# Optimization experiments

Hardware: AMD Instinct MI355X
Metric: run time of the kernel (lower is better)

## Reference

```python
import jax, jax.numpy as jnp
import numpy as np

S, B, C, H, M = 384, 8, 1024, 16, 1536
CC = C // H


def setup_inputs() -> dict:
    key = jax.random.key(0)
    ks = jax.random.split(key, 8)
    x = jax.random.normal(ks[0], (S, B, C), dtype=jnp.float32)
    pe = jax.random.normal(ks[1], (S, B, C), dtype=jnp.float32)
    memory_k = jax.random.normal(ks[2], (M, B, H, CC), dtype=jnp.float32)
    memory_v = jax.random.normal(ks[3], (M, B, H, CC), dtype=jnp.float32)
    w_qkv = jax.random.normal(ks[4], (C, 3 * C), dtype=jnp.float32) * 0.02
    b_qkv = jnp.zeros((3 * C,), dtype=jnp.float32)
    w_out = jax.random.normal(ks[5], (C, C), dtype=jnp.float32) * 0.02
    b_out = jnp.zeros((C,), dtype=jnp.float32)
    terminal = jnp.zeros((B,), dtype=bool)
    # causal mask over the new tokens: True = masked (future positions)
    content_mask = jnp.broadcast_to(
        (jnp.arange(S)[None, :] > jnp.arange(S)[:, None])[:, :, None], (S, S, B))
    padding_mask = jnp.zeros((S, B), dtype=bool)  # True = padded
    memory_length = jax.random.randint(ks[6], (B,), 0, M, dtype=jnp.int32)
    return dict(x=x, positional_encoding=pe, memory_k=memory_k, memory_v=memory_v,
                w_qkv=w_qkv, b_qkv=b_qkv, w_out=w_out, b_out=b_out,
                terminal=terminal, content_mask=content_mask,
                padding_mask=padding_mask, memory_length=memory_length)


def reference(x, positional_encoding, memory_k, memory_v, w_qkv, b_qkv,
              w_out, b_out, terminal, content_mask, padding_mask, memory_length):
    s, b, c = x.shape
    # qkv projection
    qkv = (x + positional_encoding) @ w_qkv + b_qkv          # [s,b,3c]
    q, k, v = jnp.split(qkv, 3, axis=-1)
    q = q.reshape(s, b, H, CC)
    k = k.reshape(s, b, H, CC)
    v = v.reshape(s, b, H, CC)
    # clear_memory(terminal): zero lengths for terminal episodes
    mem_len = jnp.where(terminal, 0, memory_length)          # [b]
    # ragged memory concat expressed with fixed capacity M + padding mask
    k_full = jnp.concatenate([memory_k, k], axis=0)          # [M+s,b,H,CC]
    v_full = jnp.concatenate([memory_v, v], axis=0)
    mem_pad = jnp.arange(M)[:, None] >= mem_len[None, :]     # [M,b] True=masked
    kv_pad = jnp.concatenate([mem_pad, padding_mask], axis=0)  # [M+s,b]
    mem_content = jnp.zeros((s, M, b), dtype=bool)           # memory visible to all queries
    full_content = jnp.concatenate([mem_content, content_mask], axis=1)  # [s,M+s,b]
    mask = full_content | kv_pad[None, :, :]                 # [s,M+s,b]
    # attention
    scores = jnp.einsum('sbhc,tbhc->stbh', q, k_full) * (1.0 / np.sqrt(CC))
    scores = jnp.where(mask[:, :, :, None], jnp.float32(-1e9), scores)
    p = jax.nn.softmax(scores, axis=1)                       # [s,M+s,b,h]
    out = jnp.einsum('stbh,tbhc->sbhc', p, v_full).reshape(s, b, c)
    return out @ w_out + b_out
```

## Files before the change

### kernel.cpp

```cpp
#include <hip/hip_runtime.h>
#include <math.h>

#define S_DIM 384
#define B_DIM 8
#define C_DIM 1024
#define H_DIM 16
#define M_DIM 1536
#define CC_DIM 64
#define ROWS  (S_DIM * B_DIM)
#define N3C   (3 * C_DIM)
#define NSPLIT 4

typedef unsigned short u16;
typedef short bf8v  __attribute__((ext_vector_type(8)));
typedef short bf4v  __attribute__((ext_vector_type(4)));
typedef u16   us8   __attribute__((ext_vector_type(8)));
typedef u16   us4   __attribute__((ext_vector_type(4)));
typedef float f4v   __attribute__((ext_vector_type(4)));

__device__ __forceinline__ u16 f2bf(float f) {
    unsigned u = __float_as_uint(f);
    u += 0x7fffu + ((u >> 16) & 1u);
    return (u16)(u >> 16);
}
__device__ __forceinline__ float bf2f(u16 v) {
    return __uint_as_float(((unsigned)v) << 16);
}
#if __has_builtin(__builtin_amdgcn_exp2f)
#define EX2(x) __builtin_amdgcn_exp2f(x)
#else
#define EX2(x) __expf((x) * 0.69314718056f)
#endif
#define QSCALE (0.125f * 1.44269504f)

__device__ __forceinline__ f4v mfma16x16x16bf16(bf4v a, bf4v b, f4v c) {
#if __has_builtin(__builtin_amdgcn_mfma_f32_16x16x16bf16_1k)
    return __builtin_amdgcn_mfma_f32_16x16x16bf16_1k(a, b, c, 0, 0, 0);
#else
    return c;
#endif
}

__device__ __forceinline__ void gload16(const u16* g, u16* l) {
    __builtin_amdgcn_global_load_lds(
        (const __attribute__((address_space(1))) void*)g,
        (__attribute__((address_space(3))) void*)l, 16, 0, 0);
}

__device__ __forceinline__ void tr32(const float* __restrict__ in, u16* __restrict__ out,
                                     int R, int Cc, int r0, int c0, int tid, float* sm) {
    #pragma unroll
    for (int i = 0; i < 4; i++) {
        int r = i * 8 + (tid >> 5), c = tid & 31;
        sm[r * 33 + c] = in[(size_t)(r0 + r) * Cc + c0 + c];
    }
    __syncthreads();
    #pragma unroll
    for (int i = 0; i < 4; i++) {
        int cw = i * 8 + (tid >> 5), rw = tid & 31;
        out[(size_t)(c0 + cw) * R + r0 + rw] = f2bf(sm[rw * 33 + cw]);
    }
}

__global__ __launch_bounds__(256) void prep_all(
    const float* __restrict__ x, const float* __restrict__ pe, u16* __restrict__ Abf,
    const float* __restrict__ wqkv, u16* __restrict__ Wqkvt,
    const float* __restrict__ wout, u16* __restrict__ Woutt,
    const float* __restrict__ mk, u16* __restrict__ mk_bf,
    const float* __restrict__ mv, u16* __restrict__ mv_t)
{
    __shared__ float sm[64 * 65];
    const int bid = blockIdx.x, tid = threadIdx.x;

    if (bid < 3072) {
        size_t i = ((size_t)bid * 256 + tid) * 4;
        float4 xv = *(const float4*)(x + i);
        float4 pv = *(const float4*)(pe + i);
        us4 o;
        o[0] = f2bf(xv.x + pv.x); o[1] = f2bf(xv.y + pv.y);
        o[2] = f2bf(xv.z + pv.z); o[3] = f2bf(xv.w + pv.w);
        *(us4*)(Abf + i) = o;
    } else if (bid < 6144) {
        int b2 = bid - 3072;
        tr32(wqkv, Wqkvt, C_DIM, N3C, (b2 / 96) * 32, (b2 % 96) * 32, tid, sm);
    } else if (bid < 7168) {
        int b3 = bid - 6144;
        tr32(wout, Woutt, C_DIM, C_DIM, (b3 / 32) * 32, (b3 % 32) * 32, tid, sm);
    } else if (bid < 19456) {
        int b4 = bid - 7168;
        int R = b4 * 16 + (tid >> 4);
        int c4 = (tid & 15) * 4;
        int t = R >> 7, bh = R & 127;
        float4 v = *(const float4*)&mk[(size_t)R * 64 + c4];
        us4 o;
        o[0] = f2bf(v.x); o[1] = f2bf(v.y); o[2] = f2bf(v.z); o[3] = f2bf(v.w);
        *(us4*)&mk_bf[((size_t)bh * M_DIM + t) * 64 + c4] = o;
    } else {
        int b5 = bid - 19456;
        int bh = b5 & 127;
        int t0 = (b5 >> 7) * 64;
        #pragma unroll
        for (int i = 0; i < 16; i++) {
            int r = i * 4 + (tid >> 6), c = tid & 63;
            sm[r * 65 + c] = mv[((size_t)(t0 + r) * 128 + bh) * 64 + c];
        }
        __syncthreads();
        #pragma unroll
        for (int i = 0; i < 16; i++) {
            int cc = i * 4 + (tid >> 6), tw = tid & 63;
            mv_t[((size_t)bh * 64 + cc) * M_DIM + t0 + tw] = f2bf(sm[tw * 65 + cc]);
        }
    }
}

__global__ __launch_bounds__(256) void prep_vwt(
    const u16* __restrict__ Vw, u16* __restrict__ Vwt)
{
    __shared__ u16 tile[64][66];
    const int tid = threadIdx.x;
    const int bh = blockIdx.x & 127;
    const int t0 = (blockIdx.x >> 7) * 64;
    #pragma unroll
    for (int i = 0; i < 16; i++) {
        int r = i * 4 + (tid >> 6), c = tid & 63;
        tile[r][c] = Vw[((size_t)bh * S_DIM + t0 + r) * 64 + c];
    }
    __syncthreads();
    #pragma unroll
    for (int i = 0; i < 16; i++) {
        int cc = i * 4 + (tid >> 6), tw = tid & 63;
        Vwt[((size_t)bh * 64 + cc) * S_DIM + t0 + tw] = tile[tw][cc];
    }
}

__global__ __launch_bounds__(256) void qkv_gemm(
    const u16* __restrict__ Abf, const u16* __restrict__ Wt,
    const float* __restrict__ bias,
    u16* __restrict__ Qw, u16* __restrict__ Kw, u16* __restrict__ Vw)
{
    __shared__ u16 As[128 * 64];
    __shared__ u16 Bs[64 * 64];
    const int tid = threadIdx.x;
    const int lane = tid & 63, w = tid >> 6;
    const int lr = lane & 15, quad = lane >> 4;
    const int wm = w >> 1, wn = w & 1;
    const int row0 = blockIdx.y * 128, col0 = blockIdx.x * 64;

    f4v acc[4][2];
    #pragma unroll
    for (int i = 0; i < 4; i++)
        #pragma unroll
        for (int j = 0; j < 2; j++)
            acc[i][j] = (f4v){0.f, 0.f, 0.f, 0.f};

    for (int k0 = 0; k0 < C_DIM; k0 += 64) {
        __syncthreads();
        #pragma unroll
        for (int j = 0; j < 4; j++) {
            int idx = j * 256 + tid;
            int r = idx >> 3, c = (idx & 7) ^ (r & 7);
            gload16(&Abf[(size_t)(row0 + r) * C_DIM + k0 + c * 8], &As[idx * 8]);
        }
        #pragma unroll
        for (int j = 0; j < 2; j++) {
            int idx = j * 256 + tid;
            int r = idx >> 3, c = (idx & 7) ^ (r & 7);
            gload16(&Wt[(size_t)(col0 + r) * C_DIM + k0 + c * 8], &Bs[idx * 8]);
        }
        __syncthreads();
        #pragma unroll
        for (int kh = 0; kh < 2; kh++) {
            bf8v a[4], b[2];
            #pragma unroll
            for (int mi = 0; mi < 4; mi++) {
                int row = wm * 64 + mi * 16 + lr;
                int p = (kh * 4 + quad) ^ (lr & 7);
                a[mi] = *(const bf8v*)&As[row * 64 + p * 8];
            }
            #pragma unroll
            for (int nj = 0; nj < 2; nj++) {
                int row = wn * 32 + nj * 16 + lr;
                int p = (kh * 4 + quad) ^ (lr & 7);
                b[nj] = *(const bf8v*)&Bs[row * 64 + p * 8];
            }
            #pragma unroll
            for (int mi = 0; mi < 4; mi++)
                #pragma unroll
                for (int nj = 0; nj < 2; nj++)
                    acc[mi][nj] = __builtin_amdgcn_mfma_f32_16x16x32_bf16(a[mi], b[nj], acc[mi][nj], 0, 0, 0);
        }
    }

    #pragma unroll
    for (int nj = 0; nj < 2; nj++) {
        int col = col0 + wn * 32 + nj * 16 + lr;
        float bv = bias[col];
        int which = col >> 10;
        int h = (col >> 6) & 15, cc = col & 63;
        #pragma unroll
        for (int mi = 0; mi < 4; mi++) {
            #pragma unroll
            for (int reg = 0; reg < 4; reg++) {
                int rg = row0 + wm * 64 + mi * 16 + quad * 4 + reg;
                int s = rg >> 3, bb = rg & 7;
                float v = acc[mi][nj][reg] + bv;
                size_t dst = ((size_t)((bb * 16 + h) * S_DIM) + s) * 64 + cc;
                if (which == 0)      Qw[dst] = f2bf(v * QSCALE);
                else if (which == 1) Kw[dst] = f2bf(v);
                else                 Vw[dst] = f2bf(v);
            }
        }
    }
}

__global__ __launch_bounds__(256) void attn_split(
    const u16* __restrict__ Qw, const u16* __restrict__ Kw,
    const u16* __restrict__ mk_bf, const u16* __restrict__ Vwt,
    const u16* __restrict__ mv_t, const unsigned char* __restrict__ terminal,
    const int* __restrict__ mem_len, u16* __restrict__ Op, float* __restrict__ ml)
{
    __shared__ u16 Ks[64 * 64];
    __shared__ u16 Vs[64 * 64];

    const int tid = threadIdx.x;
    const int lane = tid & 63, w = tid >> 6;
    const int lr = lane & 15, quad = lane >> 4, q8 = quad * 8;
    const int bid = blockIdx.x;
    const int split = bid & (NSPLIT - 1);
    const int g = bid / NSPLIT;
    const int b = g & 7, h = (g >> 3) & 15, sc = g >> 7;
    const int bh = b * 16 + h, sq0 = sc * 64;
    const int L = terminal[b] ? 0 : mem_len[b];
    const int qrow = sq0 + w * 16 + lr;

    const u16* qbase = Qw + ((size_t)bh * S_DIM + sq0 + w * 16 + lr) * 64;
    bf8v qf0 = *(const bf8v*)&qbase[q8];
    bf8v qf1 = *(const bf8v*)&qbase[32 + q8];

    f4v O[4];
    #pragma unroll
    for (int nj = 0; nj < 4; nj++) O[nj] = (f4v){0.f, 0.f, 0.f, 0.f};
    float m_i = -1e30f, l_i = 0.0f;

    const int memChunks = (L + 63) >> 6;
    const int total = memChunks + sc + 1;
    const int lo = (split * total) / NSPLIT;
    const int hi = ((split + 1) * total) / NSPLIT;

    const f4v zero = (f4v){0.f, 0.f, 0.f, 0.f};

    for (int ch = lo; ch < hi; ch++) {
        const bool isMem = (ch < memChunks);
        const int tloc = isMem ? ch * 64 : (ch - memChunks) * 64;
        const u16* kb = isMem ? mk_bf + ((size_t)bh * M_DIM + tloc) * 64
                              : Kw + ((size_t)bh * S_DIM + tloc) * 64;
        const u16* vb; size_t vstr;
        if (isMem) { vb = mv_t + (size_t)bh * 64 * M_DIM + tloc; vstr = M_DIM; }
        else       { vb = Vwt + (size_t)bh * 64 * S_DIM + tloc; vstr = S_DIM; }

        __syncthreads();
        #pragma unroll
        for (int j = 0; j < 2; j++) {
            int idx = j * 256 + tid;
            int r = idx >> 3, c = (idx & 7) ^ (r & 7);
            gload16(kb + (size_t)r * 64 + c * 8, &Ks[idx * 8]);
        }
        #pragma unroll
        for (int j = 0; j < 2; j++) {
            int idx = j * 256 + tid;
            int cc = idx >> 3, c = (idx & 7) ^ (cc & 7);
            gload16(vb + (size_t)cc * vstr + c * 8, &Vs[idx * 8]);
        }
        __syncthreads();

        f4v sv[4];
        #pragma unroll
        for (int tt = 0; tt < 4; tt++) {
            int row = tt * 16 + lr;
            int p0 = quad ^ (lr & 7), p1 = (4 + quad) ^ (lr & 7);
            bf8v k0 = *(const bf8v*)&Ks[row * 64 + p0 * 8];
            bf8v k1 = *(const bf8v*)&Ks[row * 64 + p1 * 8];
            sv[tt] = __builtin_amdgcn_mfma_f32_16x16x32_bf16(k0, qf0, zero, 0, 0, 0);
            sv[tt] = __builtin_amdgcn_mfma_f32_16x16x32_bf16(k1, qf1, sv[tt], 0, 0, 0);
        }

        if (isMem) {
            if (tloc + 64 > L) {
                #pragma unroll
                for (int tt = 0; tt < 4; tt++)
                    #pragma unroll
                    for (int reg = 0; reg < 4; reg++) {
                        int t = tloc + tt * 16 + quad * 4 + reg;
                        if (t >= L) sv[tt][reg] = -1e30f;
                    }
            }
        } else {
            if (tloc + 63 > sq0 + w * 16) {
                #pragma unroll
                for (int tt = 0; tt < 4; tt++)
                    #pragma unroll
                    for (int reg = 0; reg < 4; reg++) {
                        int t = tloc + tt * 16 + quad * 4 + reg;
                        if (t > qrow) sv[tt][reg] = -1e30f;
                    }
            }
        }

        float rowmax = fmaxf(fmaxf(sv[0][0], sv[0][1]), fmaxf(sv[0][2], sv[0][3]));
        #pragma unroll
        for (int tt = 1; tt < 4; tt++) {
            rowmax = fmaxf(rowmax, fmaxf(fmaxf(sv[tt][0], sv[tt][1]),
                                         fmaxf(sv[tt][2], sv[tt][3])));
        }
        rowmax = fmaxf(rowmax, __shfl_xor(rowmax, 16));
        rowmax = fmaxf(rowmax, __shfl_xor(rowmax, 32));
        float mnew = fmaxf(m_i, rowmax);
        float alpha = EX2(m_i - mnew);
        m_i = mnew;
        float sum = 0.0f;
        bf4v pf[4];
        #pragma unroll
        for (int tt = 0; tt < 4; tt++) {
            #pragma unroll
            for (int reg = 0; reg < 4; reg++) {
                float p = EX2(sv[tt][reg] - mnew);
                sum += p;
                pf[tt][reg] = (short)f2bf(p);
            }
        }
        sum += __shfl_xor(sum, 16);
        sum += __shfl_xor(sum, 32);
        l_i = l_i * alpha + sum;

        float alphaR[4];
        #pragma unroll
        for (int reg = 0; reg < 4; reg++)
            alphaR[reg] = __shfl(alpha, quad * 4 + reg);
        #pragma unroll
        for (int nj = 0; nj < 4; nj++)
            #pragma unroll
            for (int reg = 0; reg < 4; reg++)
                O[nj][reg] *= alphaR[reg];

        #pragma unroll
        for (int tt = 0; tt < 4; tt++) {
            #pragma unroll
            for (int nj = 0; nj < 4; nj++) {
                int cc = nj * 16 + lr;
                int c = (tt * 2 + (quad >> 1)) ^ (lr & 7);
                bf4v vf = *(const bf4v*)&Vs[cc * 64 + c * 8 + (quad & 1) * 4];
                O[nj] = mfma16x16x16bf16(pf[tt], vf, O[nj]);
            }
        }
    }

    const size_t pbase = (size_t)(g * NSPLIT + split) * 64;
    if (quad == 0) {
        int row = w * 16 + lr;
        float2 mlv = {m_i, l_i};
        *(float2*)&ml[(pbase + row) * 2] = mlv;
    }
    #pragma unroll
    for (int reg = 0; reg < 4; reg++) {
        int row = w * 16 + quad * 4 + reg;
        #pragma unroll
        for (int nj = 0; nj < 4; nj++)
            Op[(pbase + row) * 64 + nj * 16 + lr] = f2bf(O[nj][reg]);
    }
}

__global__ __launch_bounds__(256) void attn_combine(
    const u16* __restrict__ Op, const float* __restrict__ ml, u16* __restrict__ Obf)
{
    const int g = blockIdx.x;
    const int b = g & 7, h = (g >> 3) & 15, sc = g >> 7;
    const int tid = threadIdx.x;
    const int row = tid >> 2, c0 = (tid & 3) * 16;

    float m[NSPLIT], lv[NSPLIT];
    #pragma unroll
    for (int j = 0; j < NSPLIT; j++) {
        size_t base = (size_t)(g * NSPLIT + j) * 64 + row;
        m[j]  = ml[base * 2];
        lv[j] = ml[base * 2 + 1];
    }
    float mstar = m[0];
    #pragma unroll
    for (int j = 1; j < NSPLIT; j++) mstar = fmaxf(mstar, m[j]);
    float sc_j[NSPLIT], l = 0.0f;
    #pragma unroll
    for (int j = 0; j < NSPLIT; j++) {
        sc_j[j] = EX2(m[j] - mstar);
        l += sc_j[j] * lv[j];
    }
    float inv = 1.0f / l;

    float o[16];
    #pragma unroll
    for (int c = 0; c < 16; c++) o[c] = 0.0f;
    #pragma unroll
    for (int j = 0; j < NSPLIT; j++) {
        const u16* src = &Op[((size_t)(g * NSPLIT + j) * 64 + row) * 64 + c0];
        us8 v0 = *(const us8*)src;
        us8 v1 = *(const us8*)(src + 8);
        #pragma unroll
        for (int c = 0; c < 8; c++) {
            o[c]     += sc_j[j] * bf2f(v0[c]);
            o[c + 8] += sc_j[j] * bf2f(v1[c]);
        }
    }
    int s = sc * 64 + row;
    size_t dst = ((size_t)s * 8 + b) * C_DIM + h * 64 + c0;
    us8 w0, w1;
    #pragma unroll
    for (int c = 0; c < 8; c++) {
        w0[c] = f2bf(o[c] * inv);
        w1[c] = f2bf(o[c + 8] * inv);
    }
    *(us8*)&Obf[dst] = w0;
    *(us8*)&Obf[dst + 8] = w1;
}

__global__ __launch_bounds__(256) void proj_gemm(
    const u16* __restrict__ Abf, const u16* __restrict__ Wt,
    const float* __restrict__ bias, float* __restrict__ out)
{
    __shared__ u16 As[128 * 64];
    __shared__ u16 Bs[64 * 64];
    const int tid = threadIdx.x;
    const int lane = tid & 63, w = tid >> 6;
    const int lr = lane & 15, quad = lane >> 4;
    const int wm = w >> 1, wn = w & 1;
    const int row0 = blockIdx.y * 128, col0 = blockIdx.x * 64;

    f4v acc[4][2];
    #pragma unroll
    for (int i = 0; i < 4; i++)
        #pragma unroll
        for (int j = 0; j < 2; j++)
            acc[i][j] = (f4v){0.f, 0.f, 0.f, 0.f};

    for (int k0 = 0; k0 < C_DIM; k0 += 64) {
        __syncthreads();
        #pragma unroll
        for (int j = 0; j < 4; j++) {
            int idx = j * 256 + tid;
            int r = idx >> 3, c = (idx & 7) ^ (r & 7);
            gload16(&Abf[(size_t)(row0 + r) * C_DIM + k0 + c * 8], &As[idx * 8]);
        }
        #pragma unroll
        for (int j = 0; j < 2; j++) {
            int idx = j * 256 + tid;
            int r = idx >> 3, c = (idx & 7) ^ (r & 7);
            gload16(&Wt[(size_t)(col0 + r) * C_DIM + k0 + c * 8], &Bs[idx * 8]);
        }
        __syncthreads();
        #pragma unroll
        for (int kh = 0; kh < 2; kh++) {
            bf8v a[4], b[2];
            #pragma unroll
            for (int mi = 0; mi < 4; mi++) {
                int row = wm * 64 + mi * 16 + lr;
                int p = (kh * 4 + quad) ^ (lr & 7);
                a[mi] = *(const bf8v*)&As[row * 64 + p * 8];
            }
            #pragma unroll
            for (int nj = 0; nj < 2; nj++) {
                int row = wn * 32 + nj * 16 + lr;
                int p = (kh * 4 + quad) ^ (lr & 7);
                b[nj] = *(const bf8v*)&Bs[row * 64 + p * 8];
            }
            #pragma unroll
            for (int mi = 0; mi < 4; mi++)
                #pragma unroll
                for (int nj = 0; nj < 2; nj++)
                    acc[mi][nj] = __builtin_amdgcn_mfma_f32_16x16x32_bf16(a[mi], b[nj], acc[mi][nj], 0, 0, 0);
        }
    }

    #pragma unroll
    for (int nj = 0; nj < 2; nj++) {
        int col = col0 + wn * 32 + nj * 16 + lr;
        float bv = bias[col];
        #pragma unroll
        for (int mi = 0; mi < 4; mi++) {
            #pragma unroll
            for (int reg = 0; reg < 4; reg++) {
                int rg = row0 + wm * 64 + mi * 16 + quad * 4 + reg;
                out[(size_t)rg * C_DIM + col] = acc[mi][nj][reg] + bv;
            }
        }
    }
}

extern "C" void kernel_launch(void* const* d_in, const int* in_sizes, int n_in,
                              void* d_out, int out_size, void* d_ws, size_t ws_size,
                              hipStream_t stream) {
    const float* x    = (const float*)d_in[0];
    const float* pe   = (const float*)d_in[1];
    const float* mk   = (const float*)d_in[2];
    const float* mv   = (const float*)d_in[3];
    const float* wqkv = (const float*)d_in[4];
    const float* bqkv = (const float*)d_in[5];
    const float* wout = (const float*)d_in[6];
    const float* bout = (const float*)d_in[7];
    const unsigned char* term = (const unsigned char*)d_in[8];
    const int* mem_len = (const int*)d_in[11];

    char* ws = (char*)d_ws;
    u16* Abf   = (u16*)(ws + 0);
    u16* Obf   = (u16*)(ws + 0);
    u16* Wqkvt = (u16*)(ws + 6291456);
    u16* Vwt   = (u16*)(ws + 6291456);
    u16* Woutt = (u16*)(ws + 12582912);
    u16* mk_bf = (u16*)(ws + 14680064);
    u16* mv_t  = (u16*)(ws + 39845888);
    u16* Qw    = (u16*)(ws + 65011712);
    u16* Kw    = (u16*)(ws + 71303168);
    u16* Vw    = (u16*)(ws + 77594624);
    u16* Op    = (u16*)(ws + 83886080);
    float* ml  = (float*)(ws + 109051904);

    float* out = (float*)d_out;

    prep_all<<<22528, 256, 0, stream>>>(x, pe, Abf, wqkv, Wqkvt, wout, Woutt,
                                        mk, mk_bf, mv, mv_t);

    qkv_gemm<<<dim3(N3C / 64, ROWS / 128), 256, 0, stream>>>(
        Abf, Wqkvt, bqkv, Qw, Kw, Vw);

    prep_vwt<<<(S_DIM / 64) * 128, 256, 0, stream>>>(Vw, Vwt);

    attn_split<<<B_DIM * H_DIM * (S_DIM / 64) * NSPLIT, 256, 0, stream>>>(
        Qw, Kw, mk_bf, Vwt, mv_t, term, mem_len, Op, ml);

    attn_combine<<<B_DIM * H_DIM * (S_DIM / 64), 256, 0, stream>>>(Op, ml, Obf);

    proj_gemm<<<dim3(C_DIM / 64, ROWS / 128), 256, 0, stream>>>(
        Obf, Woutt, bout, out);
}
```

Measured before the change: 295.8 us.

## Double-buffer LDS tiles in GEMMs and attention; coarsen prep kernel blocks

The QKV and output-projection GEMMs and the split attention kernel now use two LDS buffers. The next K-tile or KV chunk is loaded with global_load_lds while the current one is being computed, which hides global-load latency behind the MFMA work. The prep kernel gives each block more work (64x64 transposes, four or eight elements per thread, two 64-row V tiles), cutting the grid from 22528 blocks to 4864. The costs are doubled LDS use, which may lower occupancy, and a larger sm array in prep_all.

```diff
diff --git a/kernel.cpp b/kernel.cpp
--- a/kernel.cpp
+++ b/kernel.cpp
@@ -47,18 +47,18 @@
         (__attribute__((address_space(3))) void*)l, 16, 0, 0);
 }
 
-__device__ __forceinline__ void tr32(const float* __restrict__ in, u16* __restrict__ out,
+__device__ __forceinline__ void tr64(const float* __restrict__ in, u16* __restrict__ out,
                                      int R, int Cc, int r0, int c0, int tid, float* sm) {
     #pragma unroll
-    for (int i = 0; i < 4; i++) {
-        int r = i * 8 + (tid >> 5), c = tid & 31;
-        sm[r * 33 + c] = in[(size_t)(r0 + r) * Cc + c0 + c];
+    for (int i = 0; i < 16; i++) {
+        int r = i * 4 + (tid >> 6), c = tid & 63;
+        sm[r * 65 + c] = in[(size_t)(r0 + r) * Cc + c0 + c];
     }
     __syncthreads();
     #pragma unroll
-    for (int i = 0; i < 4; i++) {
-        int cw = i * 8 + (tid >> 5), rw = tid & 31;
-        out[(size_t)(c0 + cw) * R + r0 + rw] = f2bf(sm[rw * 33 + cw]);
+    for (int i = 0; i < 16; i++) {
+        int cw = i * 4 + (tid >> 6), rw = tid & 63;
+        out[(size_t)(c0 + cw) * R + r0 + rw] = f2bf(sm[rw * 65 + cw]);
     }
 }
 
@@ -69,47 +69,57 @@
     const float* __restrict__ mk, u16* __restrict__ mk_bf,
     const float* __restrict__ mv, u16* __restrict__ mv_t)
 {
-    __shared__ float sm[64 * 65];
+    __shared__ float sm[2][64 * 65];
     const int bid = blockIdx.x, tid = threadIdx.x;
 
-    if (bid < 3072) {
-        size_t i = ((size_t)bid * 256 + tid) * 4;
-        float4 xv = *(const float4*)(x + i);
-        float4 pv = *(const float4*)(pe + i);
-        us4 o;
-        o[0] = f2bf(xv.x + pv.x); o[1] = f2bf(xv.y + pv.y);
-        o[2] = f2bf(xv.z + pv.z); o[3] = f2bf(xv.w + pv.w);
-        *(us4*)(Abf + i) = o;
-    } else if (bid < 6144) {
-        int b2 = bid - 3072;
-        tr32(wqkv, Wqkvt, C_DIM, N3C, (b2 / 96) * 32, (b2 % 96) * 32, tid, sm);
-    } else if (bid < 7168) {
-        int b3 = bid - 6144;
-        tr32(wout, Woutt, C_DIM, C_DIM, (b3 / 32) * 32, (b3 % 32) * 32, tid, sm);
-    } else if (bid < 19456) {
-        int b4 = bid - 7168;
-        int R = b4 * 16 + (tid >> 4);
+    if (bid < 768) {
+        size_t base = (size_t)bid * 4096 + tid * 4;
+        #pragma unroll
+        for (int j = 0; j < 4; j++) {
+            size_t i = base + j * 1024;
+            float4 xv = *(const float4*)(x + i);
+            float4 pv = *(const float4*)(pe + i);
+            us4 o;
+            o[0] = f2bf(xv.x + pv.x); o[1] = f2bf(xv.y + pv.y);
+            o[2] = f2bf(xv.z + pv.z); o[3] = f2bf(xv.w + pv.w);
+            *(us4*)(Abf + i) = o;
+        }
+    } else if (bid < 1536) {
+        int b2 = bid - 768;
+        tr64(wqkv, Wqkvt, C_DIM, N3C, (b2 / 48) * 64, (b2 % 48) * 64, tid, sm[0]);
+    } else if (bid < 1792) {
+        int b3 = bid - 1536;
+        tr64(wout, Woutt, C_DIM, C_DIM, (b3 / 16) * 64, (b3 % 16) * 64, tid, sm[0]);
+    } else if (bid < 3328) {
+        int b4 = bid - 1792;
         int c4 = (tid & 15) * 4;
-        int t = R >> 7, bh = R & 127;
-        float4 v = *(const float4*)&mk[(size_t)R * 64 + c4];
-        us4 o;
-        o[0] = f2bf(v.x); o[1] = f2bf(v.y); o[2] = f2bf(v.z); o[3] = f2bf(v.w);
-        *(us4*)&mk_bf[((size_t)bh * M_DIM + t) * 64 + c4] = o;
+        #pragma unroll
+        for (int j = 0; j < 8; j++) {
+            int R = b4 * 128 + j * 16 + (tid >> 4);
+            int t = R >> 7, bhh = R & 127;
+            float4 v = *(const float4*)&mk[(size_t)R * 64 + c4];
+            us4 o;
+            o[0] = f2bf(v.x); o[1] = f2bf(v.y); o[2] = f2bf(v.z); o[3] = f2bf(v.w);
+            *(us4*)&mk_bf[((size_t)bhh * M_DIM + t) * 64 + c4] = o;
+        }
     } else {
-        int b5 = bid - 19456;
-        int bh = b5 & 127;
-        int t0 = (b5 >> 7) * 64;
-        #pragma unroll
-        for (int i = 0; i < 16; i++) {
-            int r = i * 4 + (tid >> 6), c = tid & 63;
-            sm[r * 65 + c] = mv[((size_t)(t0 + r) * 128 + bh) * 64 + c];
-        }
+        int b5 = bid - 3328;
+        int bh = b5 & 127, t0 = (b5 >> 7) * 128;
+        #pragma unroll
+        for (int p = 0; p < 2; p++)
+            #pragma unroll
+            for (int i = 0; i < 16; i++) {
+                int r = i * 4 + (tid >> 6), c = tid & 63;
+                sm[p][r * 65 + c] = mv[((size_t)(t0 + p * 64 + r) * 128 + bh) * 64 + c];
+            }
         __syncthreads();
         #pragma unroll
-        for (int i = 0; i < 16; i++) {
-            int cc = i * 4 + (tid >> 6), tw = tid & 63;
-            mv_t[((size_t)bh * 64 + cc) * M_DIM + t0 + tw] = f2bf(sm[tw * 65 + cc]);
-        }
+        for (int p = 0; p < 2; p++)
+            #pragma unroll
+            for (int i = 0; i < 16; i++) {
+                int cc = i * 4 + (tid >> 6), tw = tid & 63;
+                mv_t[((size_t)bh * 64 + cc) * M_DIM + t0 + p * 64 + tw] = f2bf(sm[p][tw * 65 + cc]);
+            }
     }
 }
 
@@ -138,36 +148,44 @@
     const float* __restrict__ bias,
     u16* __restrict__ Qw, u16* __restrict__ Kw, u16* __restrict__ Vw)
 {
-    __shared__ u16 As[128 * 64];
-    __shared__ u16 Bs[64 * 64];
+    __shared__ u16 As[2 * 128 * 64];
+    __shared__ u16 Bs[2 * 64 * 64];
     const int tid = threadIdx.x;
     const int lane = tid & 63, w = tid >> 6;
     const int lr = lane & 15, quad = lane >> 4;
     const int wm = w >> 1, wn = w & 1;
     const int row0 = blockIdx.y * 128, col0 = blockIdx.x * 64;
 
-    f4v acc[4][2];
-    #pragma unroll
-    for (int i = 0; i < 4; i++)
-        #pragma unroll
-        for (int j = 0; j < 2; j++)
-            acc[i][j] = (f4v){0.f, 0.f, 0.f, 0.f};
-
-    for (int k0 = 0; k0 < C_DIM; k0 += 64) {
-        __syncthreads();
+    auto stage = [&](int bu, int k0) {
+        u16* Ad = &As[bu * 128 * 64];
+        u16* Bd = &Bs[bu * 64 * 64];
         #pragma unroll
         for (int j = 0; j < 4; j++) {
             int idx = j * 256 + tid;
             int r = idx >> 3, c = (idx & 7) ^ (r & 7);
-            gload16(&Abf[(size_t)(row0 + r) * C_DIM + k0 + c * 8], &As[idx * 8]);
+            gload16(&Abf[(size_t)(row0 + r) * C_DIM + k0 + c * 8], &Ad[idx * 8]);
         }
         #pragma unroll
         for (int j = 0; j < 2; j++) {
             int idx = j * 256 + tid;
             int r = idx >> 3, c = (idx & 7) ^ (r & 7);
-            gload16(&Wt[(size_t)(col0 + r) * C_DIM + k0 + c * 8], &Bs[idx * 8]);
-        }
+            gload16(&Wt[(size_t)(col0 + r) * C_DIM + k0 + c * 8], &Bd[idx * 8]);
+        }
+    };
+
+    f4v acc[4][2];
+    #pragma unroll
+    for (int i = 0; i < 4; i++)
+        #pragma unroll
+        for (int j = 0; j < 2; j++)
+            acc[i][j] = (f4v){0.f, 0.f, 0.f, 0.f};
+
+    stage(0, 0);
+    for (int ki = 0; ki < 16; ki++) {
         __syncthreads();
+        if (ki < 15) stage((ki + 1) & 1, (ki + 1) * 64);
+        const u16* Ab = &As[(ki & 1) * 128 * 64];
+        const u16* Bb = &Bs[(ki & 1) * 64 * 64];
         #pragma unroll
         for (int kh = 0; kh < 2; kh++) {
             bf8v a[4], b[2];
@@ -175,13 +193,13 @@
             for (int mi = 0; mi < 4; mi++) {
                 int row = wm * 64 + mi * 16 + lr;
                 int p = (kh * 4 + quad) ^ (lr & 7);
-                a[mi] = *(const bf8v*)&As[row * 64 + p * 8];
+                a[mi] = *(const bf8v*)&Ab[row * 64 + p * 8];
             }
             #pragma unroll
             for (int nj = 0; nj < 2; nj++) {
                 int row = wn * 32 + nj * 16 + lr;
                 int p = (kh * 4 + quad) ^ (lr & 7);
-                b[nj] = *(const bf8v*)&Bs[row * 64 + p * 8];
+                b[nj] = *(const bf8v*)&Bb[row * 64 + p * 8];
             }
             #pragma unroll
             for (int mi = 0; mi < 4; mi++)
@@ -219,8 +237,8 @@
     const u16* __restrict__ mv_t, const unsigned char* __restrict__ terminal,
     const int* __restrict__ mem_len, u16* __restrict__ Op, float* __restrict__ ml)
 {
-    __shared__ u16 Ks[64 * 64];
-    __shared__ u16 Vs[64 * 64];
+    __shared__ u16 Ks[2 * 64 * 64];
+    __shared__ u16 Vs[2 * 64 * 64];
 
     const int tid = threadIdx.x;
     const int lane = tid & 63, w = tid >> 6;
@@ -249,37 +267,50 @@
 
     const f4v zero = (f4v){0.f, 0.f, 0.f, 0.f};
 
-    for (int ch = lo; ch < hi; ch++) {
-        const bool isMem = (ch < memChunks);
-        const int tloc = isMem ? ch * 64 : (ch - memChunks) * 64;
-        const u16* kb = isMem ? mk_bf + ((size_t)bh * M_DIM + tloc) * 64
-                              : Kw + ((size_t)bh * S_DIM + tloc) * 64;
+    auto stageCh = [&](int bu, int ch) {
+        const bool isM = (ch < memChunks);
+        const int tl = isM ? ch * 64 : (ch - memChunks) * 64;
+        const u16* kb = isM ? mk_bf + ((size_t)bh * M_DIM + tl) * 64
+                            : Kw + ((size_t)bh * S_DIM + tl) * 64;
         const u16* vb; size_t vstr;
-        if (isMem) { vb = mv_t + (size_t)bh * 64 * M_DIM + tloc; vstr = M_DIM; }
-        else       { vb = Vwt + (size_t)bh * 64 * S_DIM + tloc; vstr = S_DIM; }
-
-        __syncthreads();
+        if (isM) { vb = mv_t + (size_t)bh * 64 * M_DIM + tl; vstr = M_DIM; }
+        else     { vb = Vwt + (size_t)bh * 64 * S_DIM + tl; vstr = S_DIM; }
+        u16* Kd = &Ks[bu * 64 * 64];
+        u16* Vd = &Vs[bu * 64 * 64];
         #pragma unroll
         for (int j = 0; j < 2; j++) {
             int idx = j * 256 + tid;
             int r = idx >> 3, c = (idx & 7) ^ (r & 7);
-            gload16(kb + (size_t)r * 64 + c * 8, &Ks[idx * 8]);
+            gload16(kb + (size_t)r * 64 + c * 8, &Kd[idx * 8]);
         }
         #pragma unroll
         for (int j = 0; j < 2; j++) {
             int idx = j * 256 + tid;
             int cc = idx >> 3, c = (idx & 7) ^ (cc & 7);
-            gload16(vb + (size_t)cc * vstr + c * 8, &Vs[idx * 8]);
-        }
+            gload16(vb + (size_t)cc * vstr + c * 8, &Vd[idx * 8]);
+        }
+    };
+
+    if (lo < hi) stageCh(0, lo);
+
+    for (int ch = lo; ch < hi; ch++) {
+        const int bu = (ch - lo) & 1;
+        const bool isMem = (ch < memChunks);
+        const int tloc = isMem ? ch * 64 : (ch - memChunks) * 64;
+
         __syncthreads();
+        if (ch + 1 < hi) stageCh(bu ^ 1, ch + 1);
+
+        const u16* Kb = &Ks[bu * 64 * 64];
+        const u16* Vb = &Vs[bu * 64 * 64];
 
         f4v sv[4];
         #pragma unroll
         for (int tt = 0; tt < 4; tt++) {
             int row = tt * 16 + lr;
             int p0 = quad ^ (lr & 7), p1 = (4 + quad) ^ (lr & 7);
-            bf8v k0 = *(const bf8v*)&Ks[row * 64 + p0 * 8];
-            bf8v k1 = *(const bf8v*)&Ks[row * 64 + p1 * 8];
+            bf8v k0 = *(const bf8v*)&Kb[row * 64 + p0 * 8];
+            bf8v k1 = *(const bf8v*)&Kb[row * 64 + p1 * 8];
             sv[tt] = __builtin_amdgcn_mfma_f32_16x16x32_bf16(k0, qf0, zero, 0, 0, 0);
             sv[tt] = __builtin_amdgcn_mfma_f32_16x16x32_bf16(k1, qf1, sv[tt], 0, 0, 0);
         }
@@ -308,10 +339,9 @@
 
         float rowmax = fmaxf(fmaxf(sv[0][0], sv[0][1]), fmaxf(sv[0][2], sv[0][3]));
         #pragma unroll
-        for (int tt = 1; tt < 4; tt++) {
+        for (int tt = 1; tt < 4; tt++)
             rowmax = fmaxf(rowmax, fmaxf(fmaxf(sv[tt][0], sv[tt][1]),
                                          fmaxf(sv[tt][2], sv[tt][3])));
-        }
         rowmax = fmaxf(rowmax, __shfl_xor(rowmax, 16));
         rowmax = fmaxf(rowmax, __shfl_xor(rowmax, 32));
         float mnew = fmaxf(m_i, rowmax);
@@ -348,7 +378,7 @@
             for (int nj = 0; nj < 4; nj++) {
                 int cc = nj * 16 + lr;
                 int c = (tt * 2 + (quad >> 1)) ^ (lr & 7);
-                bf4v vf = *(const bf4v*)&Vs[cc * 64 + c * 8 + (quad & 1) * 4];
+                bf4v vf = *(const bf4v*)&Vb[cc * 64 + c * 8 + (quad & 1) * 4];
                 O[nj] = mfma16x16x16bf16(pf[tt], vf, O[nj]);
             }
         }
@@ -425,36 +455,44 @@
     const u16* __restrict__ Abf, const u16* __restrict__ Wt,
     const float* __restrict__ bias, float* __restrict__ out)
 {
-    __shared__ u16 As[128 * 64];
-    __shared__ u16 Bs[64 * 64];
+    __shared__ u16 As[2 * 128 * 64];
+    __shared__ u16 Bs[2 * 64 * 64];
     const int tid = threadIdx.x;
     const int lane = tid & 63, w = tid >> 6;
     const int lr = lane & 15, quad = lane >> 4;
     const int wm = w >> 1, wn = w & 1;
     const int row0 = blockIdx.y * 128, col0 = blockIdx.x * 64;
 
-    f4v acc[4][2];
-    #pragma unroll
-    for (int i = 0; i < 4; i++)
-        #pragma unroll
-        for (int j = 0; j < 2; j++)
-            acc[i][j] = (f4v){0.f, 0.f, 0.f, 0.f};
-
-    for (int k0 = 0; k0 < C_DIM; k0 += 64) {
-        __syncthreads();
+    auto stage = [&](int bu, int k0) {
+        u16* Ad = &As[bu * 128 * 64];
+        u16* Bd = &Bs[bu * 64 * 64];
         #pragma unroll
         for (int j = 0; j < 4; j++) {
             int idx = j * 256 + tid;
             int r = idx >> 3, c = (idx & 7) ^ (r & 7);
-            gload16(&Abf[(size_t)(row0 + r) * C_DIM + k0 + c * 8], &As[idx * 8]);
+            gload16(&Abf[(size_t)(row0 + r) * C_DIM + k0 + c * 8], &Ad[idx * 8]);
         }
         #pragma unroll
         for (int j = 0; j < 2; j++) {
             int idx = j * 256 + tid;
             int r = idx >> 3, c = (idx & 7) ^ (r & 7);
-            gload16(&Wt[(size_t)(col0 + r) * C_DIM + k0 + c * 8], &Bs[idx * 8]);
-        }
+            gload16(&Wt[(size_t)(col0 + r) * C_DIM + k0 + c * 8], &Bd[idx * 8]);
+        }
+    };
+
+    f4v acc[4][2];
+    #pragma unroll
+    for (int i = 0; i < 4; i++)
+        #pragma unroll
+        for (int j = 0; j < 2; j++)
+            acc[i][j] = (f4v){0.f, 0.f, 0.f, 0.f};
+
+    stage(0, 0);
+    for (int ki = 0; ki < 16; ki++) {
         __syncthreads();
+        if (ki < 15) stage((ki + 1) & 1, (ki + 1) * 64);
+        const u16* Ab = &As[(ki & 1) * 128 * 64];
+        const u16* Bb = &Bs[(ki & 1) * 64 * 64];
         #pragma unroll
         for (int kh = 0; kh < 2; kh++) {
             bf8v a[4], b[2];
@@ -462,13 +500,13 @@
             for (int mi = 0; mi < 4; mi++) {
                 int row = wm * 64 + mi * 16 + lr;
                 int p = (kh * 4 + quad) ^ (lr & 7);
-                a[mi] = *(const bf8v*)&As[row * 64 + p * 8];
+                a[mi] = *(const bf8v*)&Ab[row * 64 + p * 8];
             }
             #pragma unroll
             for (int nj = 0; nj < 2; nj++) {
                 int row = wn * 32 + nj * 16 + lr;
                 int p = (kh * 4 + quad) ^ (lr & 7);
-                b[nj] = *(const bf8v*)&Bs[row * 64 + p * 8];
+                b[nj] = *(const bf8v*)&Bb[row * 64 + p * 8];
             }
             #pragma unroll
             for (int mi = 0; mi < 4; mi++)
@@ -523,8 +561,8 @@
 
     float* out = (float*)d_out;
 
-    prep_all<<<22528, 256, 0, stream>>>(x, pe, Abf, wqkv, Wqkvt, wout, Woutt,
-                                        mk, mk_bf, mv, mv_t);
+    prep_all<<<4864, 256, 0, stream>>>(x, pe, Abf, wqkv, Wqkvt, wout, Woutt,
+                                       mk, mk_bf, mv, mv_t);
 
     qkv_gemm<<<dim3(N3C / 64, ROWS / 128), 256, 0, stream>>>(
         Abf, Wqkvt, bqkv, Qw, Kw, Vw);
```

Result: slower. 303.9 us (+2.7%).

## Stage GEMM and attention outputs through LDS for vectorized stores; drop mk transpose

Applied to the files above, without the earlier changes.

The QKV GEMM epilogue and the attention partial-output write now go through shared memory, so each thread issues 16-byte row stores instead of scattered 2-byte stores. The memory-K conversion becomes a plain elementwise cast that keeps the original [t][bh][c] layout, and the attention kernel reads memory K with a strided row pitch instead. This cuts uncoalesced global writes in three places. In exchange it adds two extra barriers plus LDS round-trips per block, and memory-K rows are now fetched with a large stride.

```diff
diff --git a/kernel.cpp b/kernel.cpp
--- a/kernel.cpp
+++ b/kernel.cpp
@@ -88,13 +88,11 @@
         tr32(wout, Woutt, C_DIM, C_DIM, (b3 / 32) * 32, (b3 % 32) * 32, tid, sm);
     } else if (bid < 19456) {
         int b4 = bid - 7168;
-        int R = b4 * 16 + (tid >> 4);
-        int c4 = (tid & 15) * 4;
-        int t = R >> 7, bh = R & 127;
-        float4 v = *(const float4*)&mk[(size_t)R * 64 + c4];
+        size_t i = ((size_t)b4 * 256 + tid) * 4;
+        float4 v = *(const float4*)(mk + i);
         us4 o;
         o[0] = f2bf(v.x); o[1] = f2bf(v.y); o[2] = f2bf(v.z); o[3] = f2bf(v.w);
-        *(us4*)&mk_bf[((size_t)bh * M_DIM + t) * 64 + c4] = o;
+        *(us4*)(mk_bf + i) = o;
     } else {
         int b5 = bid - 19456;
         int bh = b5 & 127;
@@ -138,8 +136,11 @@
     const float* __restrict__ bias,
     u16* __restrict__ Qw, u16* __restrict__ Kw, u16* __restrict__ Vw)
 {
-    __shared__ u16 As[128 * 64];
-    __shared__ u16 Bs[64 * 64];
+    __shared__ u16 smem[128 * 64 + 64 * 64];
+    u16* As = smem;
+    u16* Bs = smem + 128 * 64;
+    u16* Cs = smem;
+
     const int tid = threadIdx.x;
     const int lane = tid & 63, w = tid >> 6;
     const int lr = lane & 15, quad = lane >> 4;
@@ -191,25 +192,31 @@
         }
     }
 
+    const int which = col0 >> 10;
+    const int h = (col0 >> 6) & 15;
+    const float qs = (which == 0) ? QSCALE : 1.0f;
+    u16* dstbuf = (which == 0) ? Qw : ((which == 1) ? Kw : Vw);
+
+    __syncthreads();
     #pragma unroll
     for (int nj = 0; nj < 2; nj++) {
         int col = col0 + wn * 32 + nj * 16 + lr;
         float bv = bias[col];
-        int which = col >> 10;
-        int h = (col >> 6) & 15, cc = col & 63;
-        #pragma unroll
-        for (int mi = 0; mi < 4; mi++) {
-            #pragma unroll
-            for (int reg = 0; reg < 4; reg++) {
-                int rg = row0 + wm * 64 + mi * 16 + quad * 4 + reg;
-                int s = rg >> 3, bb = rg & 7;
-                float v = acc[mi][nj][reg] + bv;
-                size_t dst = ((size_t)((bb * 16 + h) * S_DIM) + s) * 64 + cc;
-                if (which == 0)      Qw[dst] = f2bf(v * QSCALE);
-                else if (which == 1) Kw[dst] = f2bf(v);
-                else                 Vw[dst] = f2bf(v);
-            }
-        }
+        #pragma unroll
+        for (int mi = 0; mi < 4; mi++)
+            #pragma unroll
+            for (int reg = 0; reg < 4; reg++)
+                Cs[(wm * 64 + mi * 16 + quad * 4 + reg) * 72 + wn * 32 + nj * 16 + lr] =
+                    f2bf((acc[mi][nj][reg] + bv) * qs);
+    }
+    __syncthreads();
+    {
+        int r = tid >> 1, half = tid & 1;
+        int rg = row0 + r, s = rg >> 3, bb = rg & 7;
+        u16* drow = dstbuf + ((size_t)(bb * 16 + h) * S_DIM + s) * 64 + half * 32;
+        #pragma unroll
+        for (int i = 0; i < 4; i++)
+            *(us8*)(drow + i * 8) = *(const us8*)&Cs[r * 72 + half * 32 + i * 8];
     }
 }
 
@@ -219,8 +226,10 @@
     const u16* __restrict__ mv_t, const unsigned char* __restrict__ terminal,
     const int* __restrict__ mem_len, u16* __restrict__ Op, float* __restrict__ ml)
 {
-    __shared__ u16 Ks[64 * 64];
-    __shared__ u16 Vs[64 * 64];
+    __shared__ u16 smem[2 * 64 * 64];
+    u16* Ks = smem;
+    u16* Vs = smem + 64 * 64;
+    u16* Os = smem;
 
     const int tid = threadIdx.x;
     const int lane = tid & 63, w = tid >> 6;
@@ -252,8 +261,9 @@
     for (int ch = lo; ch < hi; ch++) {
         const bool isMem = (ch < memChunks);
         const int tloc = isMem ? ch * 64 : (ch - memChunks) * 64;
-        const u16* kb = isMem ? mk_bf + ((size_t)bh * M_DIM + tloc) * 64
-                              : Kw + ((size_t)bh * S_DIM + tloc) * 64;
+        const u16* kb; size_t kstr;
+        if (isMem) { kb = mk_bf + ((size_t)tloc * 128 + bh) * 64; kstr = 128 * 64; }
+        else       { kb = Kw + ((size_t)bh * S_DIM + tloc) * 64; kstr = 64; }
         const u16* vb; size_t vstr;
         if (isMem) { vb = mv_t + (size_t)bh * 64 * M_DIM + tloc; vstr = M_DIM; }
         else       { vb = Vwt + (size_t)bh * 64 * S_DIM + tloc; vstr = S_DIM; }
@@ -263,7 +273,7 @@
         for (int j = 0; j < 2; j++) {
             int idx = j * 256 + tid;
             int r = idx >> 3, c = (idx & 7) ^ (r & 7);
-            gload16(kb + (size_t)r * 64 + c * 8, &Ks[idx * 8]);
+            gload16(kb + (size_t)r * kstr + c * 8, &Ks[idx * 8]);
         }
         #pragma unroll
         for (int j = 0; j < 2; j++) {
@@ -308,10 +318,9 @@
 
         float rowmax = fmaxf(fmaxf(sv[0][0], sv[0][1]), fmaxf(sv[0][2], sv[0][3]));
         #pragma unroll
-        for (int tt = 1; tt < 4; tt++) {
+        for (int tt = 1; tt < 4; tt++)
             rowmax = fmaxf(rowmax, fmaxf(fmaxf(sv[tt][0], sv[tt][1]),
                                          fmaxf(sv[tt][2], sv[tt][3])));
-        }
         rowmax = fmaxf(rowmax, __shfl_xor(rowmax, 16));
         rowmax = fmaxf(rowmax, __shfl_xor(rowmax, 32));
         float mnew = fmaxf(m_i, rowmax);
@@ -360,12 +369,20 @@
         float2 mlv = {m_i, l_i};
         *(float2*)&ml[(pbase + row) * 2] = mlv;
     }
-    #pragma unroll
-    for (int reg = 0; reg < 4; reg++) {
-        int row = w * 16 + quad * 4 + reg;
+    __syncthreads();
+    #pragma unroll
+    for (int reg = 0; reg < 4; reg++)
         #pragma unroll
         for (int nj = 0; nj < 4; nj++)
-            Op[(pbase + row) * 64 + nj * 16 + lr] = f2bf(O[nj][reg]);
+            Os[(w * 16 + quad * 4 + reg) * 72 + nj * 16 + lr] = f2bf(O[nj][reg]);
+    __syncthreads();
+    {
+        int row = tid >> 2, q4 = tid & 3;
+        us8 v0 = *(const us8*)&Os[row * 72 + q4 * 16];
+        us8 v1 = *(const us8*)&Os[row * 72 + q4 * 16 + 8];
+        size_t ob = (pbase + row) * 64 + q4 * 16;
+        *(us8*)&Op[ob] = v0;
+        *(us8*)&Op[ob + 8] = v1;
     }
 }
 
```

Result: slower. 303.2 us (+2.5%).
